# Kernel tuning notes

Measured on AMD Instinct MI355X. Metric: run time of the kernel, lower is better.

The kernel has to match this reference:

```python
import jax, jax.numpy as jnp
import numpy as np

N = 2048
OUT = 16

def setup_inputs() -> dict:
    key = jax.random.key(0)
    k1, k2 = jax.random.split(key)
    inputs = jax.random.normal(k1, (N, N), dtype=jnp.float32)
    w = jax.random.normal(k2, (15, OUT), dtype=jnp.float32) * 0.05  # random_normal init
    return {"inputs": inputs, "w": w}

def reference(inputs, w):
    # inputs: [N, N], w: [15, out]
    n = inputs.shape[0]
    dt = inputs.dtype
    diag = jnp.diagonal(inputs)          # [N]
    rowsum = inputs.sum(axis=1)          # [N]  'ij->i'
    colsum = inputs.sum(axis=0)          # [N]  'ij->j'
    trace = diag.sum()
    totsum = inputs.sum()
    eye = jnp.eye(n, dtype=dt)
    ones = jnp.ones((n, n), dtype=dt)
    as_row = lambda v: jnp.broadcast_to(v[None, :], (n, n))  # ones_i * v_j -> ij
    as_col = lambda v: jnp.broadcast_to(v[:, None], (n, n))  # ones_i * v_j -> ji
    basis = jnp.stack([
        jnp.diag(diag),          # 0: diag embedded on diagonal
        jnp.diag(rowsum),        # 1
        jnp.diag(colsum),        # 2
        eye * trace,             # 3: identity * trace
        eye * totsum,            # 4: identity * totsum
        as_row(diag),            # 5: 'i,j->ij' ones, diag
        as_row(rowsum),          # 6
        as_row(colsum),          # 7
        as_col(diag),            # 8: 'i,j->ji' ones, diag
        as_col(rowsum),          # 9
        as_col(colsum),          # 10
        inputs.T,                # 11
        inputs,                  # 12
        ones * trace,            # 13
        ones * totsum,           # 14
    ], axis=-1)                  # [N, N, 15]
    # activation is identity (None)
    return jnp.einsum('ijk,ko->ijo', basis, w)  # [N, N, out]
```

## Files before the change

kernel.cpp:

```cpp
#include <hip/hip_runtime.h>

#define NMAT 2048

typedef float f32x4 __attribute__((ext_vector_type(4)));

__device__ __forceinline__ float4 f4fma(float a, float4 b, float4 c) {
    return make_float4(fmaf(a, b.x, c.x), fmaf(a, b.y, c.y),
                       fmaf(a, b.z, c.z), fmaf(a, b.w, c.w));
}
__device__ __forceinline__ float4 f4scale(float a, float4 b) {
    return make_float4(a * b.x, a * b.y, a * b.z, a * b.w);
}

__global__ __launch_bounds__(256) void k_stats(const float* __restrict__ in,
                                               float* __restrict__ rowsum,
                                               float* __restrict__ diag,
                                               float* __restrict__ colsum,
                                               float* __restrict__ scal) {
    const int t = threadIdx.x;
    const int r0 = blockIdx.x * 8;
    __shared__ float lrs[8][256];
    float4 c0 = make_float4(0.f, 0.f, 0.f, 0.f);
    float4 c1 = make_float4(0.f, 0.f, 0.f, 0.f);
#pragma unroll
    for (int r = 0; r < 8; ++r) {
        const float4* row = (const float4*)(in + (size_t)(r0 + r) * NMAT);
        float4 v0 = row[t];
        float4 v1 = row[t + 256];
        c0.x += v0.x; c0.y += v0.y; c0.z += v0.z; c0.w += v0.w;
        c1.x += v1.x; c1.y += v1.y; c1.z += v1.z; c1.w += v1.w;
        lrs[r][t] = ((v0.x + v0.y) + (v0.z + v0.w)) +
                    ((v1.x + v1.y) + (v1.z + v1.w));
    }
    atomicAdd(&colsum[4 * t + 0], c0.x);
    atomicAdd(&colsum[4 * t + 1], c0.y);
    atomicAdd(&colsum[4 * t + 2], c0.z);
    atomicAdd(&colsum[4 * t + 3], c0.w);
    atomicAdd(&colsum[1024 + 4 * t + 0], c1.x);
    atomicAdd(&colsum[1024 + 4 * t + 1], c1.y);
    atomicAdd(&colsum[1024 + 4 * t + 2], c1.z);
    atomicAdd(&colsum[1024 + 4 * t + 3], c1.w);
    __syncthreads();
    {
        const int row = t >> 5;
        const int lane = t & 31;
        float s = 0.f;
#pragma unroll
        for (int k = 0; k < 8; ++k) s += lrs[row][lane + 32 * k];
        s += __shfl_down(s, 16);
        s += __shfl_down(s, 8);
        s += __shfl_down(s, 4);
        s += __shfl_down(s, 2);
        s += __shfl_down(s, 1);
        if (lane == 0) {
            rowsum[r0 + row] = s;
            atomicAdd(&scal[1], s);
        }
    }
    if (t < 8) {
        const int r = r0 + t;
        const float d = in[(size_t)r * NMAT + r];
        diag[r] = d;
        atomicAdd(&scal[0], d);
    }
}

__global__ __launch_bounds__(256) void k_main(const float* __restrict__ in,
                                              const float* __restrict__ w,
                                              const float* __restrict__ rowsum,
                                              const float* __restrict__ diag,
                                              const float* __restrict__ colsum,
                                              const float* __restrict__ scal,
                                              float4* __restrict__ out4) {
    const int t = threadIdx.x;
    const int og = t & 3;
    const int tj = (t >> 2) & 31;
    const int half = t >> 7;
    const int j = blockIdx.x * 32 + tj;
    const int i0 = blockIdx.y * 32;
    const bool dblk = (blockIdx.x == blockIdx.y);
    const float4* W = (const float4*)w;
    const float4 w8 = W[8 * 4 + og], w9 = W[9 * 4 + og], w10 = W[10 * 4 + og];
    const float4 w11 = W[11 * 4 + og], w12 = W[12 * 4 + og];
    const float tr = scal[0], ts = scal[1];
    float4 base = f4scale(diag[j], W[5 * 4 + og]);
    base = f4fma(rowsum[j], W[6 * 4 + og], base);
    base = f4fma(colsum[j], W[7 * 4 + og], base);
    base = f4fma(tr, W[13 * 4 + og], base);
    base = f4fma(ts, W[14 * 4 + og], base);
    const size_t jrow = (size_t)j * NMAT;
#pragma unroll 8
    for (int it = 0; it < 16; ++it) {
        const int i = i0 + half + 2 * it;
        const float di = diag[i];
        const float rsi = rowsum[i];
        const float csi = colsum[i];
        const float a = in[(size_t)i * NMAT + j];
        const float at = in[jrow + i];
        float4 r = f4fma(di, w8, base);
        r = f4fma(rsi, w9, r);
        r = f4fma(csi, w10, r);
        r = f4fma(a, w12, r);
        r = f4fma(at, w11, r);
        if (dblk && i == j) {
            float4 dd = f4scale(di, W[0 * 4 + og]);
            dd = f4fma(rsi, W[1 * 4 + og], dd);
            dd = f4fma(csi, W[2 * 4 + og], dd);
            dd = f4fma(tr, W[3 * 4 + og], dd);
            dd = f4fma(ts, W[4 * 4 + og], dd);
            r.x += dd.x; r.y += dd.y; r.z += dd.z; r.w += dd.w;
        }
        f32x4 rv = {r.x, r.y, r.z, r.w};
        __builtin_nontemporal_store(
            rv, (f32x4*)&out4[((size_t)i * NMAT + j) * 4 + og]);
    }
}

extern "C" void kernel_launch(void* const* d_in, const int* in_sizes, int n_in,
                              void* d_out, int out_size, void* d_ws, size_t ws_size,
                              hipStream_t stream) {
    const float* in = (const float*)d_in[0];
    const float* w = (const float*)d_in[1];
    float* ws = (float*)d_ws;

    float* colsum = ws;
    float* scal = ws + 2048;
    float* rowsum = ws + 2056;
    float* diag = ws + 4104;

    hipMemsetAsync(d_ws, 0, 2050 * sizeof(float), stream);
    k_stats<<<256, 256, 0, stream>>>(in, rowsum, diag, colsum, scal);
    k_main<<<dim3(64, 64), 256, 0, stream>>>(in, w, rowsum, diag, colsum, scal,
                                             (float4*)d_out);
}
```

Measured before the change: 311.5 us.

## Assign one output element per thread with four float4 stores and wider tiles

Remaps the main kernel so each thread owns a full 16-wide output vector for one (i,j), iterating 16 rows per block with 256 columns per block, and keeps all weight rows in registers. Nontemporal stores are replaced by regular stores. The aim is to amortise the per-element loads and the weight setup, at the cost of strided stores across lanes, a less coalesced transpose read, and higher register pressure.

```diff
diff --git a/kernel.cpp b/kernel.cpp
--- a/kernel.cpp
+++ b/kernel.cpp
@@ -71,48 +71,62 @@
                                               const float* __restrict__ diag,
                                               const float* __restrict__ colsum,
                                               const float* __restrict__ scal,
-                                              float4* __restrict__ out4) {
+                                              float* __restrict__ out) {
     const int t = threadIdx.x;
-    const int og = t & 3;
-    const int tj = (t >> 2) & 31;
-    const int half = t >> 7;
-    const int j = blockIdx.x * 32 + tj;
-    const int i0 = blockIdx.y * 32;
-    const bool dblk = (blockIdx.x == blockIdx.y);
+    const int j = blockIdx.x * 256 + t;
+    const int i0 = blockIdx.y * 16;
     const float4* W = (const float4*)w;
-    const float4 w8 = W[8 * 4 + og], w9 = W[9 * 4 + og], w10 = W[10 * 4 + og];
-    const float4 w11 = W[11 * 4 + og], w12 = W[12 * 4 + og];
+    float4 w8[4], w9[4], w10[4], w11[4], w12[4];
+#pragma unroll
+    for (int og = 0; og < 4; ++og) {
+        w8[og] = W[8 * 4 + og];
+        w9[og] = W[9 * 4 + og];
+        w10[og] = W[10 * 4 + og];
+        w11[og] = W[11 * 4 + og];
+        w12[og] = W[12 * 4 + og];
+    }
     const float tr = scal[0], ts = scal[1];
-    float4 base = f4scale(diag[j], W[5 * 4 + og]);
-    base = f4fma(rowsum[j], W[6 * 4 + og], base);
-    base = f4fma(colsum[j], W[7 * 4 + og], base);
-    base = f4fma(tr, W[13 * 4 + og], base);
-    base = f4fma(ts, W[14 * 4 + og], base);
+    const float dj = diag[j], rsj = rowsum[j], csj = colsum[j];
+    float4 base[4];
+#pragma unroll
+    for (int og = 0; og < 4; ++og) {
+        float4 b = f4scale(dj, W[5 * 4 + og]);
+        b = f4fma(rsj, W[6 * 4 + og], b);
+        b = f4fma(csj, W[7 * 4 + og], b);
+        b = f4fma(tr, W[13 * 4 + og], b);
+        b = f4fma(ts, W[14 * 4 + og], b);
+        base[og] = b;
+    }
     const size_t jrow = (size_t)j * NMAT;
-#pragma unroll 8
-    for (int it = 0; it < 16; ++it) {
-        const int i = i0 + half + 2 * it;
+    const bool dblk = (j >= i0) && (j < i0 + 16);
+#pragma unroll 2
+    for (int ii = 0; ii < 16; ++ii) {
+        const int i = i0 + ii;
         const float di = diag[i];
         const float rsi = rowsum[i];
         const float csi = colsum[i];
         const float a = in[(size_t)i * NMAT + j];
         const float at = in[jrow + i];
-        float4 r = f4fma(di, w8, base);
-        r = f4fma(rsi, w9, r);
-        r = f4fma(csi, w10, r);
-        r = f4fma(a, w12, r);
-        r = f4fma(at, w11, r);
-        if (dblk && i == j) {
-            float4 dd = f4scale(di, W[0 * 4 + og]);
-            dd = f4fma(rsi, W[1 * 4 + og], dd);
-            dd = f4fma(csi, W[2 * 4 + og], dd);
-            dd = f4fma(tr, W[3 * 4 + og], dd);
-            dd = f4fma(ts, W[4 * 4 + og], dd);
-            r.x += dd.x; r.y += dd.y; r.z += dd.z; r.w += dd.w;
+        const bool isd = dblk && (i == j);
+        float* op = out + ((size_t)i * NMAT + j) * 16;
+#pragma unroll
+        for (int og = 0; og < 4; ++og) {
+            float4 r = f4fma(di, w8[og], base[og]);
+            r = f4fma(rsi, w9[og], r);
+            r = f4fma(csi, w10[og], r);
+            r = f4fma(a, w12[og], r);
+            r = f4fma(at, w11[og], r);
+            if (isd) {
+                float4 dd = f4scale(di, W[0 * 4 + og]);
+                dd = f4fma(rsi, W[1 * 4 + og], dd);
+                dd = f4fma(csi, W[2 * 4 + og], dd);
+                dd = f4fma(tr, W[3 * 4 + og], dd);
+                dd = f4fma(ts, W[4 * 4 + og], dd);
+                r.x += dd.x; r.y += dd.y; r.z += dd.z; r.w += dd.w;
+            }
+            f32x4 rv = {r.x, r.y, r.z, r.w};
+            *(f32x4*)(op + og * 4) = rv;
         }
-        f32x4 rv = {r.x, r.y, r.z, r.w};
-        __builtin_nontemporal_store(
-            rv, (f32x4*)&out4[((size_t)i * NMAT + j) * 4 + og]);
     }
 }
 
@@ -130,6 +144,6 @@
 
     hipMemsetAsync(d_ws, 0, 2050 * sizeof(float), stream);
     k_stats<<<256, 256, 0, stream>>>(in, rowsum, diag, colsum, scal);
-    k_main<<<dim3(64, 64), 256, 0, stream>>>(in, w, rowsum, diag, colsum, scal,
-                                             (float4*)d_out);
+    k_main<<<dim3(8, 128), 256, 0, stream>>>(in, w, rowsum, diag, colsum, scal,
+                                             (float*)d_out);
 }
```

Measured after the change: 367.5 us. 1.18x slower.

## Pre-transpose input and precompute tables for a row-linear output kernel

Applied to the files above, without the earlier changes.

Adds a shared-memory tiled transpose kernel that writes the transposed input to workspace. It also adds a small kernel that precomputes the per-column broadcast terms and the diagonal-correction terms. A new main kernel then walks one output row per block, reading the input and its transpose coalesced and writing the whole 128KB output row contiguously. This removes the strided transposed reads and scattered stores of the tiled kernel, at the cost of extra launches and about 16MB of extra transpose traffic. The old tiled path is kept as a fallback when the workspace is too small.

```diff
diff --git a/kernel.cpp b/kernel.cpp
--- a/kernel.cpp
+++ b/kernel.cpp
@@ -10,6 +10,9 @@
 }
 __device__ __forceinline__ float4 f4scale(float a, float4 b) {
     return make_float4(a * b.x, a * b.y, a * b.z, a * b.w);
+}
+__device__ __forceinline__ float4 f4add(float4 a, float4 b) {
+    return make_float4(a.x + b.x, a.y + b.y, a.z + b.z, a.w + b.w);
 }
 
 __global__ __launch_bounds__(256) void k_stats(const float* __restrict__ in,
@@ -65,13 +68,111 @@
     }
 }
 
-__global__ __launch_bounds__(256) void k_main(const float* __restrict__ in,
-                                              const float* __restrict__ w,
-                                              const float* __restrict__ rowsum,
-                                              const float* __restrict__ diag,
-                                              const float* __restrict__ colsum,
-                                              const float* __restrict__ scal,
-                                              float4* __restrict__ out4) {
+__global__ __launch_bounds__(256) void k_tr(const float* __restrict__ in,
+                                            float* __restrict__ T) {
+    __shared__ float tile[64][65];
+    const int t = threadIdx.x;
+    const int bi = blockIdx.y * 64;
+    const int bj = blockIdx.x * 64;
+    const int c4 = t & 15;
+    const int r = t >> 4;
+#pragma unroll
+    for (int s = 0; s < 4; ++s) {
+        const int row = s * 16 + r;
+        const float4 v = *(const float4*)(in + (size_t)(bi + row) * NMAT +
+                                          bj + c4 * 4);
+        tile[row][c4 * 4 + 0] = v.x;
+        tile[row][c4 * 4 + 1] = v.y;
+        tile[row][c4 * 4 + 2] = v.z;
+        tile[row][c4 * 4 + 3] = v.w;
+    }
+    __syncthreads();
+#pragma unroll
+    for (int s = 0; s < 4; ++s) {
+        const int jj = s * 16 + r;
+        float4 v;
+        v.x = tile[c4 * 4 + 0][jj];
+        v.y = tile[c4 * 4 + 1][jj];
+        v.z = tile[c4 * 4 + 2][jj];
+        v.w = tile[c4 * 4 + 3][jj];
+        *(float4*)(T + (size_t)(bj + jj) * NMAT + bi + c4 * 4) = v;
+    }
+}
+
+__global__ __launch_bounds__(256) void k_tables(const float* __restrict__ w,
+                                                const float* __restrict__ rowsum,
+                                                const float* __restrict__ diag,
+                                                const float* __restrict__ colsum,
+                                                const float* __restrict__ scal,
+                                                float4* __restrict__ B4,
+                                                float4* __restrict__ D4) {
+    const int idx = blockIdx.x * 256 + threadIdx.x;
+    const int i = idx >> 2;
+    const int og = idx & 3;
+    const float di = diag[i], rs = rowsum[i], cs = colsum[i];
+    const float tr = scal[0], ts = scal[1];
+    const float4* W = (const float4*)w;
+    float4 B = f4scale(di, W[5 * 4 + og]);
+    B = f4fma(rs, W[6 * 4 + og], B);
+    B = f4fma(cs, W[7 * 4 + og], B);
+    B = f4fma(tr, W[13 * 4 + og], B);
+    B = f4fma(ts, W[14 * 4 + og], B);
+    float4 D = f4scale(di, W[0 * 4 + og]);
+    D = f4fma(rs, W[1 * 4 + og], D);
+    D = f4fma(cs, W[2 * 4 + og], D);
+    D = f4fma(tr, W[3 * 4 + og], D);
+    D = f4fma(ts, W[4 * 4 + og], D);
+    B4[idx] = B;
+    D4[idx] = D;
+}
+
+__global__ __launch_bounds__(256) void k_main_lin(const float* __restrict__ in,
+                                                  const float* __restrict__ T,
+                                                  const float* __restrict__ w,
+                                                  const float* __restrict__ rowsum,
+                                                  const float* __restrict__ diag,
+                                                  const float* __restrict__ colsum,
+                                                  const float4* __restrict__ B4,
+                                                  const float4* __restrict__ D4,
+                                                  float4* __restrict__ out4) {
+    const int t = threadIdx.x;
+    const int og = t & 3;
+    const int jl = t >> 2;
+    const int i = blockIdx.x;
+    const float4* W = (const float4*)w;
+    const float4 w11 = W[11 * 4 + og];
+    const float4 w12 = W[12 * 4 + og];
+    const float di = diag[i], rsi = rowsum[i], csi = colsum[i];
+    float4 rt = f4scale(di, W[8 * 4 + og]);
+    rt = f4fma(rsi, W[9 * 4 + og], rt);
+    rt = f4fma(csi, W[10 * 4 + og], rt);
+    const float4 d4 = D4[i * 4 + og];
+    const float* arow = in + (size_t)i * NMAT;
+    const float* trow = T + (size_t)i * NMAT;
+    float4* orow = out4 + (size_t)i * (NMAT * 4);
+#pragma unroll 4
+    for (int p = 0; p < 32; ++p) {
+        const int j = p * 64 + jl;
+        const float a = arow[j];
+        const float at = trow[j];
+        const float4 b = B4[p * 256 + t];
+        float4 r = f4add(b, rt);
+        r = f4fma(a, w12, r);
+        r = f4fma(at, w11, r);
+        if (j == i) {
+            r.x += d4.x; r.y += d4.y; r.z += d4.z; r.w += d4.w;
+        }
+        orow[p * 256 + t] = r;
+    }
+}
+
+__global__ __launch_bounds__(256) void k_main_tiled(const float* __restrict__ in,
+                                                    const float* __restrict__ w,
+                                                    const float* __restrict__ rowsum,
+                                                    const float* __restrict__ diag,
+                                                    const float* __restrict__ colsum,
+                                                    const float* __restrict__ scal,
+                                                    float4* __restrict__ out4) {
     const int t = threadIdx.x;
     const int og = t & 3;
     const int tj = (t >> 2) & 31;
@@ -89,7 +190,7 @@
     base = f4fma(tr, W[13 * 4 + og], base);
     base = f4fma(ts, W[14 * 4 + og], base);
     const size_t jrow = (size_t)j * NMAT;
-#pragma unroll 8
+#pragma unroll 4
     for (int it = 0; it < 16; ++it) {
         const int i = i0 + half + 2 * it;
         const float di = diag[i];
@@ -127,9 +228,25 @@
     float* scal = ws + 2048;
     float* rowsum = ws + 2056;
     float* diag = ws + 4104;
+    const size_t T_OFF = 8192;
+    const size_t T_FLOATS = (size_t)NMAT * NMAT;
+    const size_t B_OFF = T_OFF + T_FLOATS;
+    const size_t D_OFF = B_OFF + 4 * 8192;
+    const size_t NEED_BYTES = (D_OFF + 4 * 8192) * sizeof(float);
 
     hipMemsetAsync(d_ws, 0, 2050 * sizeof(float), stream);
     k_stats<<<256, 256, 0, stream>>>(in, rowsum, diag, colsum, scal);
-    k_main<<<dim3(64, 64), 256, 0, stream>>>(in, w, rowsum, diag, colsum, scal,
-                                             (float4*)d_out);
-}
+
+    if (ws_size >= NEED_BYTES) {
+        float* T = ws + T_OFF;
+        float4* B4 = (float4*)(ws + B_OFF);
+        float4* D4 = (float4*)(ws + D_OFF);
+        k_tr<<<dim3(32, 32), 256, 0, stream>>>(in, T);
+        k_tables<<<32, 256, 0, stream>>>(w, rowsum, diag, colsum, scal, B4, D4);
+        k_main_lin<<<2048, 256, 0, stream>>>(in, T, w, rowsum, diag, colsum,
+                                             B4, D4, (float4*)d_out);
+    } else {
+        k_main_tiled<<<dim3(64, 64), 256, 0, stream>>>(
+            in, w, rowsum, diag, colsum, scal, (float4*)d_out);
+    }
+}
```

After: 333.7 us. +7.1%, slower.
